# Optimization experiments

Hardware: AMD Instinct MI355X
Metric: run time of the kernel (lower is better)

The kernel has to match this reference:

```python
import jax, jax.numpy as jnp
import numpy as np

B, T, D, C = 8, 4096, 768, 2048

def setup_inputs() -> dict:
    key = jax.random.key(0)
    k1, k2 = jax.random.split(key)
    embed = jax.random.normal(k1, (B, T, D), dtype=jnp.float32)
    cluster_centers = jax.random.normal(k2, (C, D), dtype=jnp.float32)
    return {"embed": embed, "cluster_centers": cluster_centers}

def reference(embed, cluster_centers):
    x_sq = jnp.sum(embed * embed, axis=-1, keepdims=True)          # (b, t, 1)
    c_sq = jnp.sum(cluster_centers * cluster_centers, axis=-1)     # (c,)
    cross = jnp.einsum('btd,cd->btc', embed, cluster_centers)      # (b, t, c)
    sq_dists = x_sq + c_sq[None, None, :] - 2.0 * cross
    dists = jnp.sqrt(jnp.maximum(sq_dists, 0.0))
    # dists argmax of -cdist == argmin of cdist
    clusters = jnp.argmin(dists, axis=-1)                          # (b, t) int
    return clusters
```

## Files before the change

kernel.cpp:

```cpp
#include <hip/hip_runtime.h>

typedef __fp16 f16x2 __attribute__((ext_vector_type(2)));
typedef __fp16 f16x8 __attribute__((ext_vector_type(8)));
typedef float f32x4 __attribute__((ext_vector_type(4)));

constexpr int MM = 32768;
constexpr int NN = 2048;
constexpr int KK = 768;
constexpr int BM = 128;
constexpr int BN = 128;
constexpr int BK = 32;

__global__ __launch_bounds__(256)
void init_ws_kernel(unsigned long long* __restrict__ w) {
    w[blockIdx.x * 256 + threadIdx.x] = 0xFFFFFFFFFFFFFFFFull;
}

__global__ __launch_bounds__(64)
void csq_kernel(const float* __restrict__ cc, float* __restrict__ csq) {
    const int cl = blockIdx.x;
    const int lane = threadIdx.x;
    const float4* row = reinterpret_cast<const float4*>(cc + (size_t)cl * KK);
    float s = 0.f;
#pragma unroll
    for (int w = 0; w < KK / (4 * 64); ++w) {
        float4 v = row[w * 64 + lane];
        s = fmaf(v.x, v.x, s); s = fmaf(v.y, v.y, s);
        s = fmaf(v.z, v.z, s); s = fmaf(v.w, v.w, s);
    }
#pragma unroll
    for (int off = 32; off > 0; off >>= 1) s += __shfl_xor(s, off, 64);
    if (lane == 0) csq[cl] = s;
}

__device__ __forceinline__ unsigned bc(f16x2 h) {
    return __builtin_bit_cast(unsigned, h);
}

__global__ __launch_bounds__(256, 2)
void argmin_mfma_kernel(const float* __restrict__ A, const float* __restrict__ Bc,
                        const float* __restrict__ csq,
                        unsigned long long* __restrict__ ws64) {
    __shared__ unsigned lds[4 * 128 * 20];
    constexpr int AH = 0, AL = 2560, BH = 5120;

    const int tid  = threadIdx.x;
    const int lane = tid & 63;
    const int ln15 = lane & 15;
    const int quad = lane >> 4;
    const int wave = tid >> 6;
    const int wm = wave >> 1, wn = wave & 1;
    const int tbase = blockIdx.x * BM;
    const int cb    = blockIdx.y * BN;

    const int sr  = tid >> 1;
    const int skh = tid & 1;
    const float* gA = A  + (size_t)(tbase + sr) * KK + skh * 16;
    const float* gB = Bc + (size_t)(cb   + sr) * KK + skh * 16;
    const int wword = sr * 20 + skh * 8;

    f32x4 acc[4][4];
#pragma unroll
    for (int i = 0; i < 4; ++i)
#pragma unroll
        for (int j = 0; j < 4; ++j) { f32x4 z = {0.f,0.f,0.f,0.f}; acc[i][j] = z; }

    float4 av[4], bv[4];
#pragma unroll
    for (int p = 0; p < 4; ++p) {
        av[p] = *(const float4*)(gA + p * 4);
        bv[p] = *(const float4*)(gB + p * 4);
    }

    int aw[4], bw[4];
#pragma unroll
    for (int i = 0; i < 4; ++i) {
        aw[i] = AH + (wm * 64 + i * 16 + ln15) * 20 + quad * 4;
        bw[i] = BH + (wn * 64 + i * 16 + ln15) * 20 + quad * 4;
    }

    for (int k0 = 0; k0 < KK; k0 += BK) {
        __syncthreads();
#pragma unroll
        for (int h = 0; h < 2; ++h) {
            float4 v0 = av[2*h], v1 = av[2*h+1];
            f16x2 h00 = __builtin_amdgcn_cvt_pkrtz(v0.x, v0.y);
            f16x2 h01 = __builtin_amdgcn_cvt_pkrtz(v0.z, v0.w);
            f16x2 h10 = __builtin_amdgcn_cvt_pkrtz(v1.x, v1.y);
            f16x2 h11 = __builtin_amdgcn_cvt_pkrtz(v1.z, v1.w);
            f16x2 l00 = __builtin_amdgcn_cvt_pkrtz(v0.x-(float)h00[0], v0.y-(float)h00[1]);
            f16x2 l01 = __builtin_amdgcn_cvt_pkrtz(v0.z-(float)h01[0], v0.w-(float)h01[1]);
            f16x2 l10 = __builtin_amdgcn_cvt_pkrtz(v1.x-(float)h10[0], v1.y-(float)h10[1]);
            f16x2 l11 = __builtin_amdgcn_cvt_pkrtz(v1.z-(float)h11[0], v1.w-(float)h11[1]);
            uint4 hv = {bc(h00), bc(h01), bc(h10), bc(h11)};
            uint4 lv = {bc(l00), bc(l01), bc(l10), bc(l11)};
            *(uint4*)&lds[AH + wword + 4*h] = hv;
            *(uint4*)&lds[AL + wword + 4*h] = lv;

            float4 w0 = bv[2*h], w1 = bv[2*h+1];
            f16x2 g00 = __builtin_amdgcn_cvt_pkrtz(w0.x, w0.y);
            f16x2 g01 = __builtin_amdgcn_cvt_pkrtz(w0.z, w0.w);
            f16x2 g10 = __builtin_amdgcn_cvt_pkrtz(w1.x, w1.y);
            f16x2 g11 = __builtin_amdgcn_cvt_pkrtz(w1.z, w1.w);
            f16x2 m00 = __builtin_amdgcn_cvt_pkrtz(w0.x-(float)g00[0], w0.y-(float)g00[1]);
            f16x2 m01 = __builtin_amdgcn_cvt_pkrtz(w0.z-(float)g01[0], w0.w-(float)g01[1]);
            f16x2 m10 = __builtin_amdgcn_cvt_pkrtz(w1.x-(float)g10[0], w1.y-(float)g10[1]);
            f16x2 m11 = __builtin_amdgcn_cvt_pkrtz(w1.z-(float)g11[0], w1.w-(float)g11[1]);
            uint4 gv = {bc(g00), bc(g01), bc(g10), bc(g11)};
            uint4 mv = {bc(m00), bc(m01), bc(m10), bc(m11)};
            *(uint4*)&lds[BH + wword + 4*h]        = gv;
            *(uint4*)&lds[BH + 2560 + wword + 4*h] = mv;
        }
        __syncthreads();

        const int kn = k0 + BK;
        if (kn < KK) {
#pragma unroll
            for (int p = 0; p < 4; ++p) {
                av[p] = *(const float4*)(gA + kn + p * 4);
                bv[p] = *(const float4*)(gB + kn + p * 4);
            }
        }

        f16x8 a_h[4], a_l[4], b_h[4], b_l[4];
#pragma unroll
        for (int i = 0; i < 4; ++i) {
            a_h[i] = *(const f16x8*)&lds[aw[i]];
            a_l[i] = *(const f16x8*)&lds[aw[i] + 2560];
            b_h[i] = *(const f16x8*)&lds[bw[i]];
            b_l[i] = *(const f16x8*)&lds[bw[i] + 2560];
        }
#pragma unroll
        for (int i = 0; i < 4; ++i)
#pragma unroll
            for (int j = 0; j < 4; ++j) {
                acc[i][j] = __builtin_amdgcn_mfma_f32_16x16x32_f16(a_h[i], b_h[j], acc[i][j], 0, 0, 0);
                acc[i][j] = __builtin_amdgcn_mfma_f32_16x16x32_f16(a_h[i], b_l[j], acc[i][j], 0, 0, 0);
                acc[i][j] = __builtin_amdgcn_mfma_f32_16x16x32_f16(a_l[i], b_h[j], acc[i][j], 0, 0, 0);
            }
    }

    float csq4[4];
#pragma unroll
    for (int j = 0; j < 4; ++j) csq4[j] = csq[cb + wn * 64 + j * 16 + ln15];

    float bval[16]; int bidx[16];
#pragma unroll
    for (int i = 0; i < 4; ++i)
#pragma unroll
        for (int r = 0; r < 4; ++r) {
            const int rid = i * 4 + r;
            float bv_ = csq4[0] - 2.0f * acc[i][0][r];
            int   bi_ = cb + wn * 64 + ln15;
#pragma unroll
            for (int j = 1; j < 4; ++j) {
                const float s = csq4[j] - 2.0f * acc[i][j][r];
                const int   c = cb + wn * 64 + j * 16 + ln15;
                if (s < bv_) { bv_ = s; bi_ = c; }
            }
            bval[rid] = bv_; bidx[rid] = bi_;
        }

#pragma unroll
    for (int off = 1; off < 16; off <<= 1) {
#pragma unroll
        for (int rid = 0; rid < 16; ++rid) {
            const float ov = __shfl_xor(bval[rid], off, 64);
            const int   oi = __shfl_xor(bidx[rid], off, 64);
            if (ov < bval[rid] || (ov == bval[rid] && oi < bidx[rid])) {
                bval[rid] = ov; bidx[rid] = oi;
            }
        }
    }

    __syncthreads();
    float* vtab = (float*)&lds[0];
    int*   itab = (int*)&lds[256];
    if (ln15 == 0) {
#pragma unroll
        for (int i = 0; i < 4; ++i)
#pragma unroll
            for (int r = 0; r < 4; ++r) {
                const int row = wm * 64 + i * 16 + quad * 4 + r;
                vtab[row * 2 + wn] = bval[i * 4 + r];
                itab[row * 2 + wn] = bidx[i * 4 + r];
            }
    }
    __syncthreads();
    if (tid < 128) {
        float v0 = vtab[tid * 2]; int i0 = itab[tid * 2];
        const float v1 = vtab[tid * 2 + 1]; const int i1 = itab[tid * 2 + 1];
        if (v1 < v0 || (v1 == v0 && i1 < i0)) { v0 = v1; i0 = i1; }
        const unsigned b   = __float_as_uint(v0);
        const unsigned key = (b & 0x80000000u) ? ~b : (b | 0x80000000u);
        const unsigned long long pk =
            ((unsigned long long)key << 32) | (unsigned long long)(unsigned)i0;
        atomicMin(&ws64[tbase + tid], pk);
    }
}

__global__ __launch_bounds__(256)
void unpack_kernel(const unsigned long long* __restrict__ w, int* __restrict__ out) {
    const int i = blockIdx.x * 256 + threadIdx.x;
    out[i] = (int)(unsigned)(w[i] & 0xFFFFFFFFull);
}

extern "C" void kernel_launch(void* const* d_in, const int* in_sizes, int n_in,
                              void* d_out, int out_size, void* d_ws, size_t ws_size,
                              hipStream_t stream) {
    const float* embed   = (const float*)d_in[0];
    const float* centers = (const float*)d_in[1];
    int* out = (int*)d_out;
    unsigned long long* ws64 = (unsigned long long*)d_ws;
    float* csq = (float*)((char*)d_ws + (size_t)MM * 8);

    init_ws_kernel<<<MM / 256, 256, 0, stream>>>(ws64);
    csq_kernel<<<NN, 64, 0, stream>>>(centers, csq);
    argmin_mfma_kernel<<<dim3(MM / BM, NN / BN), 256, 0, stream>>>(embed, centers, csq, ws64);
    unpack_kernel<<<MM / 256, 256, 0, stream>>>(ws64, out);
}
```

Before: 447.6 us.

## Preconvert inputs to split fp16 in workspace and replace atomics with slot reduction

Adds a preconvert pass that splits embed and centers into hi/lo fp16 arrays in workspace and computes center norms in the same pass. The GEMM then loads fp16 directly instead of converting fp32 in every tile, which removes the repeated conversion work across the 16 column blocks. Per-block argmin results go to per-row slots and are reduced by a separate kernel, replacing the 64-bit atomicMin and init pass. The cost is an extra full pass over the inputs to write about 100MB of fp16 data, and the path needs a large workspace, otherwise it falls back to the old kernels.

```diff
diff --git a/kernel.cpp b/kernel.cpp
--- a/kernel.cpp
+++ b/kernel.cpp
@@ -10,6 +10,217 @@
 constexpr int BM = 128;
 constexpr int BN = 128;
 constexpr int BK = 32;
+constexpr int RSTR = KK * 2 / 16;
+
+constexpr size_t WS_AH   = 0;
+constexpr size_t WS_AL   = WS_AH + (size_t)MM * KK * 2;
+constexpr size_t WS_BH   = WS_AL + (size_t)MM * KK * 2;
+constexpr size_t WS_BL   = WS_BH + (size_t)NN * KK * 2;
+constexpr size_t WS_CSQ  = WS_BL + (size_t)NN * KK * 2;
+constexpr size_t WS_SLOT = WS_CSQ + (size_t)NN * 4;
+constexpr size_t WS_NEED = WS_SLOT + (size_t)MM * 16 * 8;
+
+__device__ __forceinline__ unsigned bc(f16x2 h) {
+    return __builtin_bit_cast(unsigned, h);
+}
+
+
+__global__ __launch_bounds__(256)
+void preconvert_kernel(const float* __restrict__ A, const float* __restrict__ Bc,
+                       unsigned short* __restrict__ AhG, unsigned short* __restrict__ AlG,
+                       unsigned short* __restrict__ BhG, unsigned short* __restrict__ BlG,
+                       float* __restrict__ csq) {
+    const int bid = blockIdx.x;
+    const bool isB = bid >= (MM / 32);
+    const int rowbase = (isB ? bid - MM / 32 : bid) * 32;
+    const int tid = threadIdx.x;
+    const int row = tid >> 3, kc = tid & 7;
+    const size_t base = (size_t)(rowbase + row) * KK + kc * 8;
+    const float* src = (isB ? Bc : A) + base;
+    unsigned short* dh = (isB ? BhG : AhG) + base;
+    unsigned short* dl = (isB ? BlG : AlG) + base;
+
+    float s = 0.f;
+#pragma unroll
+    for (int t = 0; t < 12; ++t) {
+        float4 v0 = *(const float4*)(src + t * 64);
+        float4 v1 = *(const float4*)(src + t * 64 + 4);
+        if (isB) {
+            s = fmaf(v0.x, v0.x, s); s = fmaf(v0.y, v0.y, s);
+            s = fmaf(v0.z, v0.z, s); s = fmaf(v0.w, v0.w, s);
+            s = fmaf(v1.x, v1.x, s); s = fmaf(v1.y, v1.y, s);
+            s = fmaf(v1.z, v1.z, s); s = fmaf(v1.w, v1.w, s);
+        }
+        f16x2 h0 = __builtin_amdgcn_cvt_pkrtz(v0.x, v0.y);
+        f16x2 h1 = __builtin_amdgcn_cvt_pkrtz(v0.z, v0.w);
+        f16x2 h2 = __builtin_amdgcn_cvt_pkrtz(v1.x, v1.y);
+        f16x2 h3 = __builtin_amdgcn_cvt_pkrtz(v1.z, v1.w);
+        f16x2 l0 = __builtin_amdgcn_cvt_pkrtz(v0.x-(float)h0[0], v0.y-(float)h0[1]);
+        f16x2 l1 = __builtin_amdgcn_cvt_pkrtz(v0.z-(float)h1[0], v0.w-(float)h1[1]);
+        f16x2 l2 = __builtin_amdgcn_cvt_pkrtz(v1.x-(float)h2[0], v1.y-(float)h2[1]);
+        f16x2 l3 = __builtin_amdgcn_cvt_pkrtz(v1.z-(float)h3[0], v1.w-(float)h3[1]);
+        uint4 hv = {bc(h0), bc(h1), bc(h2), bc(h3)};
+        uint4 lv = {bc(l0), bc(l1), bc(l2), bc(l3)};
+        *(uint4*)(dh + t * 64) = hv;
+        *(uint4*)(dl + t * 64) = lv;
+    }
+    if (isB) {
+        s += __shfl_xor(s, 1, 64);
+        s += __shfl_xor(s, 2, 64);
+        s += __shfl_xor(s, 4, 64);
+        if (kc == 0) csq[rowbase + row] = s;
+    }
+}
+
+__global__ __launch_bounds__(256, 2)
+void gemm_f16_kernel(const unsigned short* __restrict__ AhG, const unsigned short* __restrict__ AlG,
+                     const unsigned short* __restrict__ BhG, const unsigned short* __restrict__ BlG,
+                     const float* __restrict__ csq, uint2* __restrict__ slots) {
+    __shared__ unsigned lds[4 * 128 * 20];
+    constexpr int AH = 0, AL = 2560, BH = 5120, BL = 7680;
+
+    const int tid  = threadIdx.x;
+    const int lane = tid & 63;
+    const int ln15 = lane & 15;
+    const int quad = lane >> 4;
+    const int wave = tid >> 6;
+    const int wm = wave >> 1, wn = wave & 1;
+    const int tbase = blockIdx.x * BM;
+    const int cb    = blockIdx.y * BN;
+
+    const int r0 = tid >> 2, ku = tid & 3;
+    const uint4* gAh = (const uint4*)AhG;
+    const uint4* gAl = (const uint4*)AlG;
+    const uint4* gBh = (const uint4*)BhG;
+    const uint4* gBl = (const uint4*)BlG;
+    const size_t arow0 = (size_t)(tbase + r0) * RSTR + ku;
+    const size_t arow1 = (size_t)(tbase + r0 + 64) * RSTR + ku;
+    const size_t brow0 = (size_t)(cb + r0) * RSTR + ku;
+    const size_t brow1 = (size_t)(cb + r0 + 64) * RSTR + ku;
+    const int sw0 = r0 * 20 + ku * 4;
+    const int sw1 = sw0 + 64 * 20;
+
+    f32x4 acc[4][4];
+#pragma unroll
+    for (int i = 0; i < 4; ++i)
+#pragma unroll
+        for (int j = 0; j < 4; ++j) { f32x4 z = {0.f,0.f,0.f,0.f}; acc[i][j] = z; }
+
+    uint4 pAh0 = gAh[arow0], pAh1 = gAh[arow1];
+    uint4 pAl0 = gAl[arow0], pAl1 = gAl[arow1];
+    uint4 pBh0 = gBh[brow0], pBh1 = gBh[brow1];
+    uint4 pBl0 = gBl[brow0], pBl1 = gBl[brow1];
+
+    int aw[4], bw[4];
+#pragma unroll
+    for (int i = 0; i < 4; ++i) {
+        aw[i] = AH + (wm * 64 + i * 16 + ln15) * 20 + quad * 4;
+        bw[i] = BH + (wn * 64 + i * 16 + ln15) * 20 + quad * 4;
+    }
+
+    for (int kt = 0; kt < KK / BK; ++kt) {
+        __syncthreads();
+        *(uint4*)&lds[AH + sw0] = pAh0; *(uint4*)&lds[AH + sw1] = pAh1;
+        *(uint4*)&lds[AL + sw0] = pAl0; *(uint4*)&lds[AL + sw1] = pAl1;
+        *(uint4*)&lds[BH + sw0] = pBh0; *(uint4*)&lds[BH + sw1] = pBh1;
+        *(uint4*)&lds[BL + sw0] = pBl0; *(uint4*)&lds[BL + sw1] = pBl1;
+        __syncthreads();
+
+        if (kt + 1 < KK / BK) {
+            const size_t ko = (size_t)(kt + 1) * 4;
+            pAh0 = gAh[arow0 + ko]; pAh1 = gAh[arow1 + ko];
+            pAl0 = gAl[arow0 + ko]; pAl1 = gAl[arow1 + ko];
+            pBh0 = gBh[brow0 + ko]; pBh1 = gBh[brow1 + ko];
+            pBl0 = gBl[brow0 + ko]; pBl1 = gBl[brow1 + ko];
+        }
+
+        f16x8 a_h[4], a_l[4], b_h[4], b_l[4];
+#pragma unroll
+        for (int i = 0; i < 4; ++i) {
+            a_h[i] = *(const f16x8*)&lds[aw[i]];
+            a_l[i] = *(const f16x8*)&lds[aw[i] + (AL - AH)];
+            b_h[i] = *(const f16x8*)&lds[bw[i]];
+            b_l[i] = *(const f16x8*)&lds[bw[i] + (BL - BH)];
+        }
+#pragma unroll
+        for (int i = 0; i < 4; ++i)
+#pragma unroll
+            for (int j = 0; j < 4; ++j) {
+                acc[i][j] = __builtin_amdgcn_mfma_f32_16x16x32_f16(a_h[i], b_h[j], acc[i][j], 0, 0, 0);
+                acc[i][j] = __builtin_amdgcn_mfma_f32_16x16x32_f16(a_h[i], b_l[j], acc[i][j], 0, 0, 0);
+                acc[i][j] = __builtin_amdgcn_mfma_f32_16x16x32_f16(a_l[i], b_h[j], acc[i][j], 0, 0, 0);
+            }
+    }
+
+    float csq4[4];
+#pragma unroll
+    for (int j = 0; j < 4; ++j) csq4[j] = csq[cb + wn * 64 + j * 16 + ln15];
+
+    float bval[16]; int bidx[16];
+#pragma unroll
+    for (int i = 0; i < 4; ++i)
+#pragma unroll
+        for (int r = 0; r < 4; ++r) {
+            const int rid = i * 4 + r;
+            float bv_ = csq4[0] - 2.0f * acc[i][0][r];
+            int   bi_ = cb + wn * 64 + ln15;
+#pragma unroll
+            for (int j = 1; j < 4; ++j) {
+                const float s = csq4[j] - 2.0f * acc[i][j][r];
+                const int   c = cb + wn * 64 + j * 16 + ln15;
+                if (s < bv_) { bv_ = s; bi_ = c; }
+            }
+            bval[rid] = bv_; bidx[rid] = bi_;
+        }
+#pragma unroll
+    for (int off = 1; off < 16; off <<= 1) {
+#pragma unroll
+        for (int rid = 0; rid < 16; ++rid) {
+            const float ov = __shfl_xor(bval[rid], off, 64);
+            const int   oi = __shfl_xor(bidx[rid], off, 64);
+            if (ov < bval[rid] || (ov == bval[rid] && oi < bidx[rid])) {
+                bval[rid] = ov; bidx[rid] = oi;
+            }
+        }
+    }
+
+    __syncthreads();
+    float* vtab = (float*)&lds[0];
+    int*   itab = (int*)&lds[256];
+    if (ln15 == 0) {
+#pragma unroll
+        for (int i = 0; i < 4; ++i)
+#pragma unroll
+            for (int r = 0; r < 4; ++r) {
+                const int row = wm * 64 + i * 16 + quad * 4 + r;
+                vtab[row * 2 + wn] = bval[i * 4 + r];
+                itab[row * 2 + wn] = bidx[i * 4 + r];
+            }
+    }
+    __syncthreads();
+    if (tid < 128) {
+        float v0 = vtab[tid * 2]; int i0 = itab[tid * 2];
+        const float v1 = vtab[tid * 2 + 1]; const int i1 = itab[tid * 2 + 1];
+        if (v1 < v0 || (v1 == v0 && i1 < i0)) { v0 = v1; i0 = i1; }
+        uint2 e; e.x = __float_as_uint(v0); e.y = (unsigned)i0;
+        slots[(size_t)(tbase + tid) * 16 + blockIdx.y] = e;
+    }
+}
+
+__global__ __launch_bounds__(256)
+void slot_reduce_kernel(const uint2* __restrict__ slots, int* __restrict__ out) {
+    const int t = blockIdx.x * 256 + threadIdx.x;
+    const uint2* s = slots + (size_t)t * 16;
+    float bv = __uint_as_float(s[0].x); int bi = (int)s[0].y;
+#pragma unroll
+    for (int j = 1; j < 16; ++j) {
+        const uint2 e = s[j];
+        const float v = __uint_as_float(e.x);
+        if (v < bv || (v == bv && (int)e.y < bi)) { bv = v; bi = (int)e.y; }
+    }
+    out[t] = bi;
+}
+
 
 __global__ __launch_bounds__(256)
 void init_ws_kernel(unsigned long long* __restrict__ w) {
@@ -31,10 +242,6 @@
 #pragma unroll
     for (int off = 32; off > 0; off >>= 1) s += __shfl_xor(s, off, 64);
     if (lane == 0) csq[cl] = s;
-}
-
-__device__ __forceinline__ unsigned bc(f16x2 h) {
-    return __builtin_bit_cast(unsigned, h);
 }
 
 __global__ __launch_bounds__(256, 2)
@@ -160,7 +367,6 @@
             }
             bval[rid] = bv_; bidx[rid] = bi_;
         }
-
 #pragma unroll
     for (int off = 1; off < 16; off <<= 1) {
 #pragma unroll
@@ -211,11 +417,26 @@
     const float* embed   = (const float*)d_in[0];
     const float* centers = (const float*)d_in[1];
     int* out = (int*)d_out;
-    unsigned long long* ws64 = (unsigned long long*)d_ws;
-    float* csq = (float*)((char*)d_ws + (size_t)MM * 8);
-
-    init_ws_kernel<<<MM / 256, 256, 0, stream>>>(ws64);
-    csq_kernel<<<NN, 64, 0, stream>>>(centers, csq);
-    argmin_mfma_kernel<<<dim3(MM / BM, NN / BN), 256, 0, stream>>>(embed, centers, csq, ws64);
-    unpack_kernel<<<MM / 256, 256, 0, stream>>>(ws64, out);
-}
+
+    if (ws_size >= WS_NEED) {
+        unsigned short* Ah = (unsigned short*)((char*)d_ws + WS_AH);
+        unsigned short* Al = (unsigned short*)((char*)d_ws + WS_AL);
+        unsigned short* Bh = (unsigned short*)((char*)d_ws + WS_BH);
+        unsigned short* Bl = (unsigned short*)((char*)d_ws + WS_BL);
+        float* csq   = (float*)((char*)d_ws + WS_CSQ);
+        uint2* slots = (uint2*)((char*)d_ws + WS_SLOT);
+        preconvert_kernel<<<MM / 32 + NN / 32, 256, 0, stream>>>(
+            embed, centers, Ah, Al, Bh, Bl, csq);
+        gemm_f16_kernel<<<dim3(MM / BM, NN / BN), 256, 0, stream>>>(
+            Ah, Al, Bh, Bl, csq, slots);
+        slot_reduce_kernel<<<MM / 256, 256, 0, stream>>>(slots, out);
+    } else {
+        unsigned long long* ws64 = (unsigned long long*)d_ws;
+        float* csq = (float*)((char*)d_ws + (size_t)MM * 8);
+        init_ws_kernel<<<MM / 256, 256, 0, stream>>>(ws64);
+        csq_kernel<<<NN, 64, 0, stream>>>(centers, csq);
+        argmin_mfma_kernel<<<dim3(MM / BM, NN / BN), 256, 0, stream>>>(
+            embed, centers, csq, ws64);
+        unpack_kernel<<<MM / 256, 256, 0, stream>>>(ws64, out);
+    }
+}
```

Result: slower. 495.0 us (+10.6%).
